# Kernel optimization log

Hardware: AMD Instinct MI355X
Metric: run time of the kernel (lower is better)

The kernel has to match this reference:

```python
import jax, jax.numpy as jnp
import numpy as np

HEAD_DIM = 64
GRID = 4
DS = 4
EPS = 1e-6


def conv1x1(x, w, b):
    # x: (B,C,H,W), w: (O,C), b: (O,)
    return jnp.einsum('bchw,oc->bohw', x, w) + b[None, :, None, None]


def setup_inputs() -> dict:
    key = jax.random.key(0)
    ks = jax.random.split(key, 12)
    B, N, C = 16, 4096, 256
    s = 0.02
    return {
        'x': jax.random.normal(ks[0], (B, N, C), dtype=jnp.float32),
        'w_qkv': s * jax.random.normal(ks[1], (3 * C, C), dtype=jnp.float32),
        'b_qkv': jnp.zeros((3 * C,), dtype=jnp.float32),
        'w_q': s * jax.random.normal(ks[2], (C, C), dtype=jnp.float32),
        'b_q': jnp.zeros((C,), dtype=jnp.float32),
        'w_kv': s * jax.random.normal(ks[3], (2 * C, C), dtype=jnp.float32),
        'b_kv': jnp.zeros((2 * C,), dtype=jnp.float32),
        'w_proj': s * jax.random.normal(ks[4], (C, C), dtype=jnp.float32),
        'b_proj': jnp.zeros((C,), dtype=jnp.float32),
        'gn_w': jnp.ones((C,), dtype=jnp.float32),
        'gn_b': jnp.zeros((C,), dtype=jnp.float32),
    }


def reference(x, w_qkv, b_qkv, w_q, b_q, w_kv, b_kv, w_proj, b_proj, gn_w, gn_b):
    B, N, C = x.shape
    H = W = int(np.sqrt(N))
    hd = HEAD_DIM
    nh = C // hd
    gs = GRID
    scale = hd ** -0.5

    xi = x.transpose(0, 2, 1).reshape(B, C, H, W)
    qkv = conv1x1(xi, w_qkv, b_qkv)  # (B,3C,H,W)

    # ---- grid-window attention (gs x gs windows) ----
    gh, gw = H // gs, W // gs
    qkv = qkv.reshape(B, 3, nh, hd, gh, gs, gw, gs)
    qkv = qkv.transpose(1, 0, 2, 4, 6, 5, 7, 3).reshape(3, -1, gs * gs, hd)
    q, k, v = qkv[0], qkv[1], qkv[2]  # (B*nh*gh*gw, gs*gs, hd)
    attn = jax.nn.softmax(jnp.einsum('wqd,wkd->wqk', q, k) * scale, axis=-1)
    grid_x = jnp.einsum('wqk,wkd->wqd', attn, v)
    grid_x = grid_x.reshape(B, nh, gh, gw, gs, gs, hd)
    grid_x = grid_x.transpose(0, 1, 6, 2, 4, 3, 5).reshape(B, C, H, W)

    # channels_first LayerNorm(x + grid_x)
    z = xi + grid_x
    u = z.mean(1, keepdims=True)
    s2 = ((z - u) ** 2).mean(1, keepdims=True)
    grid_x = gn_w[None, :, None, None] * ((z - u) / jnp.sqrt(s2 + EPS)) + gn_b[None, :, None, None]

    # ---- pooled global attention ----
    qg = conv1x1(grid_x, w_q, b_q).reshape(B, nh, hd, N).transpose(0, 1, 3, 2)  # (B,nh,N,hd)
    pooled = grid_x.reshape(B, C, H // DS, DS, W // DS, DS).mean(axis=(3, 5))
    kv = conv1x1(pooled, w_kv, b_kv).reshape(B, 2, nh, hd, -1).transpose(1, 0, 2, 4, 3)
    k, v = kv[0], kv[1]  # (B,nh,Np,hd)
    attn = jax.nn.softmax(jnp.einsum('bhqd,bhkd->bhqk', qg, k) * scale, axis=-1)
    global_x = jnp.einsum('bhqk,bhkd->bhqd', attn, v)
    global_x = global_x.transpose(0, 1, 3, 2).reshape(B, C, H, W) + grid_x

    out = conv1x1(global_x, w_proj, b_proj)
    return out.reshape(B, C, N).transpose(0, 2, 1)
```

## Files before the change

### kernel.cpp

```cpp
#include <hip/hip_runtime.h>
#include <cstddef>

#define SCALE 0.125f
#define LN_EPS 1e-6f

typedef __attribute__((ext_vector_type(8))) short bf16x8;
typedef __attribute__((ext_vector_type(4))) float f32x4;

__device__ __forceinline__ unsigned short f2bf(float f) {
    unsigned u = __float_as_uint(f);
    return (unsigned short)((u + 0x7FFFu + ((u >> 16) & 1u)) >> 16);
}
__device__ __forceinline__ unsigned pack2(float a, float b) {
    return (unsigned)f2bf(a) | ((unsigned)f2bf(b) << 16);
}
__device__ __forceinline__ float bflo(unsigned v) { return __uint_as_float(v << 16); }
__device__ __forceinline__ float bfhi(unsigned v) { return __uint_as_float(v & 0xFFFF0000u); }
__device__ __forceinline__ float bf2f(short s) { return __uint_as_float(((unsigned)(unsigned short)s) << 16); }

#define GLOAD16(gp, lp) __builtin_amdgcn_global_load_lds( \
    (const __attribute__((address_space(1))) void*)(gp),  \
    (__attribute__((address_space(3))) void*)(lp), 16, 0, 0)

__global__ __launch_bounds__(256) void k_castw(
    const float* __restrict__ wqkv, const float* __restrict__ wq,
    const float* __restrict__ wkv, const float* __restrict__ wproj,
    short* __restrict__ wb)
{
    const int blk = blockIdx.x;
    const float* src; size_t so, doff;
    if (blk < 96)       { src = wqkv;  so = (size_t)blk * 2048;         doff = 0; }
    else if (blk < 128) { src = wq;    so = (size_t)(blk - 96) * 2048;  doff = 196608; }
    else if (blk < 192) { src = wkv;   so = (size_t)(blk - 128) * 2048; doff = 262144; }
    else                { src = wproj; so = (size_t)(blk - 192) * 2048; doff = 393216; }
    const size_t idx = so + (size_t)threadIdx.x * 8;
    const float4 f0 = *(const float4*)(src + idx);
    const float4 f1 = *(const float4*)(src + idx + 4);
    uint4 o;
    o.x = pack2(f0.x, f0.y); o.y = pack2(f0.z, f0.w);
    o.z = pack2(f1.x, f1.y); o.w = pack2(f1.z, f1.w);
    *(uint4*)(wb + doff + idx) = o;
}

__global__ __launch_bounds__(256) void k_castx(
    const float* __restrict__ x, short* __restrict__ xb)
{
    const size_t i = ((size_t)blockIdx.x * 256 + threadIdx.x) * 8;
    const float4 f0 = *(const float4*)(x + i);
    const float4 f1 = *(const float4*)(x + i + 4);
    uint4 o;
    o.x = pack2(f0.x, f0.y); o.y = pack2(f0.z, f0.w);
    o.z = pack2(f1.x, f1.y); o.w = pack2(f1.z, f1.w);
    *(uint4*)(xb + i) = o;
}

template<int OUTMODE>
__global__ __launch_bounds__(256, 4) void k_gemm(
    const short* __restrict__ Asrc, const short* __restrict__ Bw,
    const float* __restrict__ bias, void* __restrict__ Cdst,
    short* __restrict__ Vdst, int ldc, int nbn)
{
    __shared__ short Sh[17408];
    short* const As0 = Sh;
    short* const Bs0 = Sh + 8192;

    const int tid = threadIdx.x;
    const int q8 = gridDim.x >> 3;
    const int bid = (blockIdx.x & 7) * q8 + (blockIdx.x >> 3);
    const int bm = bid / nbn, bn = bid % nbn;
    const size_t m0 = (size_t)bm * 128, n0 = (size_t)bn * 128;
    const int wid = tid >> 6, lane = tid & 63;
    const int wr = wid >> 1, wc = wid & 1;
    const int g = lane >> 4, r = lane & 15;
    const int rowc = lane >> 3, gran = lane & 7;

    f32x4 acc[4][4];
    #pragma unroll
    for (int mi = 0; mi < 4; ++mi)
        #pragma unroll
        for (int nj = 0; nj < 4; ++nj) acc[mi][nj] = (f32x4)0.f;

    auto STAGE = [&](int kt) {
        const int k0 = kt * 64;
        #pragma unroll
        for (int i = 0; i < 4; ++i) {
            const int rbase = wid * 32 + i * 8;
            const int row = rbase + rowc;
            const int sg = gran ^ (row & 7);
            GLOAD16(Asrc + (m0 + row) * 256 + k0 + sg * 8, As0 + rbase * 64);
            GLOAD16(Bw   + (n0 + row) * 256 + k0 + sg * 8, Bs0 + rbase * 64);
        }
    };

    auto COMPUTE = [&]() {
        #pragma unroll
        for (int ks = 0; ks < 2; ++ks) {
            const int ke = ks * 32 + g * 8;
            bf16x8 a[4], b[4];
            #pragma unroll
            for (int mi = 0; mi < 4; ++mi) {
                const int row = wr * 64 + mi * 16 + r;
                a[mi] = *(const bf16x8*)&As0[row * 64 + (ke ^ ((row & 7) << 3))];
            }
            #pragma unroll
            for (int nj = 0; nj < 4; ++nj) {
                const int row = wc * 64 + nj * 16 + r;
                b[nj] = *(const bf16x8*)&Bs0[row * 64 + (ke ^ ((row & 7) << 3))];
            }
            #pragma unroll
            for (int mi = 0; mi < 4; ++mi)
                #pragma unroll
                for (int nj = 0; nj < 4; ++nj)
                    acc[mi][nj] = __builtin_amdgcn_mfma_f32_16x16x32_bf16(
                        a[mi], b[nj], acc[mi][nj], 0, 0, 0);
        }
    };

    #pragma unroll
    for (int kt = 0; kt < 4; ++kt) {
        STAGE(kt);
        __syncthreads();
        COMPUTE();
        __syncthreads();
    }

    if (OUTMODE == 1) {
        short* const Cl = Sh;
        #pragma unroll
        for (int nj = 0; nj < 4; ++nj) {
            const int col = wc * 64 + nj * 16 + r;
            const float bv = bias[n0 + col];
            #pragma unroll
            for (int mi = 0; mi < 4; ++mi) {
                const int row = wr * 64 + mi * 16 + g * 4;
                #pragma unroll
                for (int e = 0; e < 4; ++e)
                    Cl[(row + e) * 136 + col] = (short)f2bf(acc[mi][nj][e] + bv);
            }
        }
        __syncthreads();
        short* C = (short*)Cdst;
        #pragma unroll
        for (int j = 0; j < 8; ++j) {
            const int row = j * 16 + (tid >> 4);
            const int c8 = (tid & 15) * 8;
            const uint4 v = *(const uint4*)&Cl[row * 136 + c8];
            *(uint4*)(C + (m0 + row) * ldc + n0 + c8) = v;
        }
    } else {
        #pragma unroll
        for (int nj = 0; nj < 4; ++nj) {
            const size_t col = n0 + wc * 64 + nj * 16 + r;
            const float bv = bias[col];
            #pragma unroll
            for (int mi = 0; mi < 4; ++mi) {
                const size_t row = m0 + wr * 64 + mi * 16 + g * 4;
                #pragma unroll
                for (int e = 0; e < 4; ++e) {
                    const float v = acc[mi][nj][e] + bv;
                    const size_t rr = row + e;
                    if (OUTMODE == 0) ((float*)Cdst)[rr * ldc + col] = v;
                    else {
                        const int colk = (int)col - 256;
                        if (colk < 0) ((short*)Cdst)[rr * 256 + col] = (short)f2bf(v);
                        else {
                            const int hh = colk >> 6, dd = colk & 63;
                            Vdst[((((rr >> 8) * 4 + hh) * 64 + dd) << 8) + (rr & 255)] = (short)f2bf(v);
                        }
                    }
                }
            }
        }
    }
}

__global__ __launch_bounds__(256) void k_vtr(
    const short* __restrict__ qkvb, short* __restrict__ vwb)
{
    __shared__ short Vl[16][260];
    const int tid = threadIdx.x;
    const int blk = blockIdx.x;
    const int b = blk >> 8, win = blk & 255;
    const int ghi = win >> 4, gwi = win & 15;
    const size_t nb = (size_t)b * 4096;

    #pragma unroll
    for (int i = 0; i < 2; ++i) {
        const int c = i * 256 + tid;
        const int tok = c >> 5, ch = c & 31;
        const int n = (ghi * 4 + (tok >> 2)) * 64 + gwi * 4 + (tok & 3);
        const uint4 u = *(const uint4*)(qkvb + (nb + n) * 768 + 512 + ch * 8);
        short* dst = &Vl[tok][ch * 8];
        *(uint2*)dst = make_uint2(u.x, u.y);
        *(uint2*)(dst + 4) = make_uint2(u.z, u.w);
    }
    __syncthreads();

    unsigned w[8];
    #pragma unroll
    for (int k = 0; k < 8; ++k) {
        const unsigned lo = (unsigned)(unsigned short)Vl[2 * k][tid];
        const unsigned hi = (unsigned)(unsigned short)Vl[2 * k + 1][tid];
        w[k] = lo | (hi << 16);
    }
    short* dst = vwb + ((size_t)blk * 256 + tid) * 16;
    *(uint4*)dst = make_uint4(w[0], w[1], w[2], w[3]);
    *(uint4*)(dst + 8) = make_uint4(w[4], w[5], w[6], w[7]);
}

__global__ __launch_bounds__(256) void k_win3(
    const short* __restrict__ qkvb, const short* __restrict__ vwb,
    const short* __restrict__ xb, const float* __restrict__ gnw,
    const float* __restrict__ gnb, short* __restrict__ lnb,
    short* __restrict__ pooledb)
{
    __shared__ float zbuf[16][260];
    __shared__ short Pb[4][16][40];

    const int tid = threadIdx.x;
    const int blk = blockIdx.x;
    const int b = blk >> 8, win = blk & 255;
    const int ghi = win >> 4, gwi = win & 15;
    const size_t nb = (size_t)b * 4096;
    const int h = tid >> 6, lane = tid & 63;
    const int g = lane >> 4, l15 = lane & 15;

    const int n15 = (ghi * 4 + (l15 >> 2)) * 64 + gwi * 4 + (l15 & 3);
    const size_t qkrow = (nb + n15) * 768;
    const bf16x8 aq0 = *(const bf16x8*)(qkvb + qkrow + h * 64 + g * 8);
    const bf16x8 aq1 = *(const bf16x8*)(qkvb + qkrow + h * 64 + 32 + g * 8);
    const bf16x8 bk0 = *(const bf16x8*)(qkvb + qkrow + 256 + h * 64 + g * 8);
    const bf16x8 bk1 = *(const bf16x8*)(qkvb + qkrow + 256 + h * 64 + 32 + g * 8);

    f32x4 acc = (f32x4)0.f;
    acc = __builtin_amdgcn_mfma_f32_16x16x32_bf16(aq0, bk0, acc, 0, 0, 0);
    acc = __builtin_amdgcn_mfma_f32_16x16x32_bf16(aq1, bk1, acc, 0, 0, 0);

    float p[4];
    #pragma unroll
    for (int e = 0; e < 4; ++e) {
        const float s = acc[e] * SCALE;
        float mm = s;
        mm = fmaxf(mm, __shfl_xor(mm, 1)); mm = fmaxf(mm, __shfl_xor(mm, 2));
        mm = fmaxf(mm, __shfl_xor(mm, 4)); mm = fmaxf(mm, __shfl_xor(mm, 8));
        const float pe = __expf(s - mm);
        float rs = pe;
        rs += __shfl_xor(rs, 1); rs += __shfl_xor(rs, 2);
        rs += __shfl_xor(rs, 4); rs += __shfl_xor(rs, 8);
        p[e] = pe / rs;
    }
    #pragma unroll
    for (int e = 0; e < 4; ++e) {
        Pb[h][g * 4 + e][l15] = (short)f2bf(p[e]);
        Pb[h][g * 4 + e][16 + l15] = 0;
    }
    __syncthreads();

    const bf16x8 ap = *(const bf16x8*)&Pb[h][l15][g * 8];
    f32x4 oc[4];
    #pragma unroll
    for (int nt = 0; nt < 4; ++nt) oc[nt] = (f32x4)0.f;
    const short* vbase = vwb + ((((size_t)b * 256 + win) * 4 + h) << 10);
    #pragma unroll
    for (int nt = 0; nt < 4; ++nt) {
        const bf16x8 bv = *(const bf16x8*)(vbase + (nt * 16 + l15) * 16 + g * 8);
        oc[nt] = __builtin_amdgcn_mfma_f32_16x16x32_bf16(ap, bv, oc[nt], 0, 0, 0);
    }
    #pragma unroll
    for (int e = 0; e < 4; ++e)
        #pragma unroll
        for (int nt = 0; nt < 4; ++nt)
            zbuf[g * 4 + e][h * 64 + nt * 16 + l15] = oc[nt][e];
    __syncthreads();

    {
        const float4 gw = ((const float4*)gnw)[lane];
        const float4 gb = ((const float4*)gnb)[lane];
        #pragma unroll
        for (int i = 0; i < 4; ++i) {
            const int t = h * 4 + i;
            const int n = (ghi * 4 + (t >> 2)) * 64 + gwi * 4 + (t & 3);
            float4 zv = *(const float4*)&zbuf[t][lane * 4];
            const short4 xv = *(const short4*)(xb + (nb + n) * 256 + lane * 4);
            zv.x += bf2f(xv.x); zv.y += bf2f(xv.y);
            zv.z += bf2f(xv.z); zv.w += bf2f(xv.w);
            float ssum = zv.x + zv.y + zv.z + zv.w;
            for (int off = 1; off < 64; off <<= 1) ssum += __shfl_xor(ssum, off);
            const float u = ssum * (1.f / 256.f);
            const float dx = zv.x - u, dy = zv.y - u, dz = zv.z - u, dw = zv.w - u;
            float vsum = dx * dx + dy * dy + dz * dz + dw * dw;
            for (int off = 1; off < 64; off <<= 1) vsum += __shfl_xor(vsum, off);
            const float rinv = rsqrtf(vsum * (1.f / 256.f) + LN_EPS);
            float4 y;
            y.x = gw.x * dx * rinv + gb.x;
            y.y = gw.y * dy * rinv + gb.y;
            y.z = gw.z * dz * rinv + gb.z;
            y.w = gw.w * dw * rinv + gb.w;
            *(float4*)&zbuf[t][lane * 4] = y;
            short4 sv;
            sv.x = (short)f2bf(y.x); sv.y = (short)f2bf(y.y);
            sv.z = (short)f2bf(y.z); sv.w = (short)f2bf(y.w);
            *(short4*)(lnb + (nb + n) * 256 + lane * 4) = sv;
        }
    }
    __syncthreads();

    {
        float ps = 0.f;
        #pragma unroll
        for (int t = 0; t < 16; ++t) ps += zbuf[t][tid];
        pooledb[((size_t)b * 256 + win) * 256 + tid] = (short)f2bf(ps * (1.f / 16.f));
    }
}

#define CP 136
__global__ __launch_bounds__(512, 4) void k_glb(
    const short* __restrict__ qgb, const short* __restrict__ kb,
    const short* __restrict__ vtb, const short* __restrict__ lnb,
    short* __restrict__ gxb)
{
    __shared__ short Ks[128 * 64];
    __shared__ short Vt[64 * 128];
    __shared__ short Pl[8][16 * CP];

    const int tid = threadIdx.x;
    const int bid = (blockIdx.x & 7) * 256 + (blockIdx.x >> 3);
    const int bh = bid >> 5, qt = bid & 31;
    const int b = bh >> 2, h = bh & 3;
    const int q0 = qt * 128;
    const size_t nb = (size_t)b * 4096;

    const int w = tid >> 6, lane = tid & 63;
    const int g = lane >> 4, l15 = lane & 15;

    bf16x8 aq[2];
    {
        const int n = q0 + w * 16 + l15;
        const short* qp = qgb + (nb + n) * 256 + h * 64 + g * 8;
        aq[0] = *(const bf16x8*)qp;
        aq[1] = *(const bf16x8*)(qp + 32);
    }

    f32x4 oc[4];
    #pragma unroll
    for (int nt = 0; nt < 4; ++nt) oc[nt] = (f32x4)0.f;
    float rs[4] = {0.f, 0.f, 0.f, 0.f};

    const short* ksrc = kb + ((size_t)b * 256) * 256 + h * 64;
    const short* vsrc = vtb + (size_t)bh * 16384;
    short* Pw = &Pl[w][0];

    for (int c = 0; c < 2; ++c) {
        if (c) __syncthreads();
        #pragma unroll
        for (int i = 0; i < 2; ++i) {
            const int cc = i * 512 + tid;
            const int p = cc >> 3, d8 = (cc & 7) * 8;
            const uint4 u = *(const uint4*)(ksrc + (size_t)(c * 128 + p) * 256 + d8);
            *(uint4*)&Ks[p * 64 + (d8 ^ ((p & 7) << 3))] = u;
        }
        #pragma unroll
        for (int i = 0; i < 2; ++i) {
            const int cc = i * 512 + tid;
            const int d = cc >> 4, k8 = (cc & 15) * 8;
            const uint4 u = *(const uint4*)(vsrc + d * 256 + c * 128 + k8);
            *(uint4*)&Vt[d * 128 + (k8 ^ ((d & 7) << 3))] = u;
        }
        __syncthreads();

        f32x4 acc[8];
        #pragma unroll
        for (int nt = 0; nt < 8; ++nt) acc[nt] = (f32x4)0.f;
        #pragma unroll
        for (int nt = 0; nt < 8; ++nt) {
            const int key = nt * 16 + l15;
            const int sw = (key & 7) << 3;
            const bf16x8 bk0 = *(const bf16x8*)&Ks[key * 64 + ((g * 8) ^ sw)];
            const bf16x8 bk1 = *(const bf16x8*)&Ks[key * 64 + ((g * 8 + 32) ^ sw)];
            acc[nt] = __builtin_amdgcn_mfma_f32_16x16x32_bf16(aq[0], bk0, acc[nt], 0, 0, 0);
            acc[nt] = __builtin_amdgcn_mfma_f32_16x16x32_bf16(aq[1], bk1, acc[nt], 0, 0, 0);
        }

        #pragma unroll
        for (int e = 0; e < 4; ++e) {
            const int prow = (g * 4 + e) * CP;
            float rsum = 0.f;
            #pragma unroll
            for (int nt = 0; nt < 8; ++nt) {
                const float p = __expf(acc[nt][e] * SCALE);
                rsum += p;
                Pw[prow + nt * 16 + l15] = (short)f2bf(p);
            }
            rs[e] += rsum;
        }

        #pragma unroll
        for (int ks = 0; ks < 4; ++ks) {
            const int kc = ks * 32 + g * 8;
            const bf16x8 a0 = *(const bf16x8*)&Pw[l15 * CP + kc];
            #pragma unroll
            for (int nt = 0; nt < 4; ++nt) {
                const int d = nt * 16 + l15;
                const bf16x8 bv = *(const bf16x8*)&Vt[d * 128 + (kc ^ ((d & 7) << 3))];
                oc[nt] = __builtin_amdgcn_mfma_f32_16x16x32_bf16(a0, bv, oc[nt], 0, 0, 0);
            }
        }
    }

    #pragma unroll
    for (int e = 0; e < 4; ++e) {
        float v = rs[e];
        v += __shfl_xor(v, 1); v += __shfl_xor(v, 2);
        v += __shfl_xor(v, 4); v += __shfl_xor(v, 8);
        rs[e] = v;
    }

    #pragma unroll
    for (int e = 0; e < 4; ++e) {
        const float inv = 1.f / rs[e];
        const int n = q0 + w * 16 + g * 4 + e;
        const size_t base = (nb + n) * 256 + h * 64;
        #pragma unroll
        for (int nt = 0; nt < 4; ++nt) {
            const int d = nt * 16 + l15;
            gxb[base + d] = (short)f2bf(oc[nt][e] * inv + bf2f(lnb[base + d]));
        }
    }
}

extern "C" void kernel_launch(void* const* d_in, const int* in_sizes, int n_in,
                              void* d_out, int out_size, void* d_ws, size_t ws_size,
                              hipStream_t stream)
{
    (void)in_sizes; (void)n_in; (void)out_size; (void)ws_size;
    const float* x     = (const float*)d_in[0];
    const float* wqkv  = (const float*)d_in[1];
    const float* bqkv  = (const float*)d_in[2];
    const float* wq    = (const float*)d_in[3];
    const float* bq    = (const float*)d_in[4];
    const float* wkv   = (const float*)d_in[5];
    const float* bkv   = (const float*)d_in[6];
    const float* wproj = (const float*)d_in[7];
    const float* bproj = (const float*)d_in[8];
    const float* gnw   = (const float*)d_in[9];
    const float* gnb   = (const float*)d_in[10];
    float* out = (float*)d_out;

    char* wsb = (char*)d_ws;
    short* wb      = (short*)(wsb + 0);
    short* qkvb    = (short*)(wsb + 1048576);
    short* lnb     = (short*)(wsb + 101711872);
    short* qgb     = (short*)(wsb + 135266304);
    short* kb      = (short*)(wsb + 168820736);
    short* vtb     = (short*)(wsb + 170917888);
    short* pooledb = (short*)(wsb + 173015040);
    short* gxb     = (short*)(wsb + 175112192);
    short* vwb     = gxb;
    short* xb      = (short*)(wsb + 208666624);

    k_castw<<<dim3(224),  dim3(256), 0, stream>>>(wqkv, wq, wkv, wproj, wb);
    k_castx<<<dim3(8192), dim3(256), 0, stream>>>(x, xb);
    k_gemm<1><<<dim3(3072), dim3(256), 0, stream>>>(xb, wb, bqkv, qkvb, nullptr, 768, 6);
    k_vtr<<<dim3(4096), dim3(256), 0, stream>>>(qkvb, vwb);
    k_win3<<<dim3(4096), dim3(256), 0, stream>>>(qkvb, vwb, xb, gnw, gnb, lnb, pooledb);
    k_gemm<1><<<dim3(1024), dim3(256), 0, stream>>>(lnb, wb + 196608, bq, qgb, nullptr, 256, 2);
    k_gemm<2><<<dim3(128), dim3(256), 0, stream>>>(pooledb, wb + 262144, bkv, kb, vtb, 512, 4);
    k_glb<<<dim3(2048), dim3(512), 0, stream>>>(qgb, kb, vtb, lnb, gxb);
    k_gemm<0><<<dim3(1024), dim3(256), 0, stream>>>(gxb, wb + 393216, bproj, out, nullptr, 256, 2);
}
```

Baseline: 193.3 us.

## Alias K and P tiles in LDS, use direct global-to-LDS loads, raise occupancy

The global attention kernel now places the P staging buffer in the same LDS region as the K tile, with an extra barrier after QK^T so the two can share space. This cuts LDS use enough to raise the occupancy hint from 4 to 6 blocks per CU. K and V tiles are loaded with global_load_lds, applying the XOR swizzle on the source address, and the softmax uses exp2 with a prescaled constant and truncates to bf16 instead of rounding. The extra barrier, the truncation-based rounding, and register pressure at higher occupancy are the trade-offs.

```diff
diff --git a/kernel.cpp b/kernel.cpp
--- a/kernel.cpp
+++ b/kernel.cpp
@@ -2,6 +2,7 @@
 #include <cstddef>
 
 #define SCALE 0.125f
+#define S2E 0.18033688011112042f
 #define LN_EPS 1e-6f
 
 typedef __attribute__((ext_vector_type(8))) short bf16x8;
@@ -314,14 +315,15 @@
 }
 
 #define CP 136
-__global__ __launch_bounds__(512, 4) void k_glb(
+__global__ __launch_bounds__(512, 6) void k_glb(
     const short* __restrict__ qgb, const short* __restrict__ kb,
     const short* __restrict__ vtb, const short* __restrict__ lnb,
     short* __restrict__ gxb)
 {
-    __shared__ short Ks[128 * 64];
-    __shared__ short Vt[64 * 128];
-    __shared__ short Pl[8][16 * CP];
+    __shared__ short Sh2[8192 + 17408];
+    short* const Vt = Sh2;
+    short* const Ks = Sh2 + 8192;
+    short* const Pl = Sh2 + 8192;
 
     const int tid = threadIdx.x;
     const int bid = (blockIdx.x & 7) * 256 + (blockIdx.x >> 3);
@@ -332,6 +334,7 @@
 
     const int w = tid >> 6, lane = tid & 63;
     const int g = lane >> 4, l15 = lane & 15;
+    const int wbase = tid & ~63;
 
     bf16x8 aq[2];
     {
@@ -348,23 +351,25 @@
 
     const short* ksrc = kb + ((size_t)b * 256) * 256 + h * 64;
     const short* vsrc = vtb + (size_t)bh * 16384;
-    short* Pw = &Pl[w][0];
+    short* Pw = Pl + w * (16 * CP);
 
     for (int c = 0; c < 2; ++c) {
         if (c) __syncthreads();
         #pragma unroll
         for (int i = 0; i < 2; ++i) {
             const int cc = i * 512 + tid;
-            const int p = cc >> 3, d8 = (cc & 7) * 8;
-            const uint4 u = *(const uint4*)(ksrc + (size_t)(c * 128 + p) * 256 + d8);
-            *(uint4*)&Ks[p * 64 + (d8 ^ ((p & 7) << 3))] = u;
+            const int p = cc >> 3;
+            const int sg = (cc & 7) ^ (p & 7);
+            GLOAD16(ksrc + (size_t)(c * 128 + p) * 256 + sg * 8,
+                    Ks + (i * 512 + wbase) * 8);
         }
         #pragma unroll
         for (int i = 0; i < 2; ++i) {
             const int cc = i * 512 + tid;
-            const int d = cc >> 4, k8 = (cc & 15) * 8;
-            const uint4 u = *(const uint4*)(vsrc + d * 256 + c * 128 + k8);
-            *(uint4*)&Vt[d * 128 + (k8 ^ ((d & 7) << 3))] = u;
+            const int d = cc >> 4;
+            const int sl = (cc & 15) ^ (d & 7);
+            GLOAD16(vsrc + d * 256 + c * 128 + sl * 8,
+                    Vt + (i * 512 + wbase) * 8);
         }
         __syncthreads();
 
@@ -380,6 +385,7 @@
             acc[nt] = __builtin_amdgcn_mfma_f32_16x16x32_bf16(aq[0], bk0, acc[nt], 0, 0, 0);
             acc[nt] = __builtin_amdgcn_mfma_f32_16x16x32_bf16(aq[1], bk1, acc[nt], 0, 0, 0);
         }
+        __syncthreads();
 
         #pragma unroll
         for (int e = 0; e < 4; ++e) {
@@ -387,9 +393,9 @@
             float rsum = 0.f;
             #pragma unroll
             for (int nt = 0; nt < 8; ++nt) {
-                const float p = __expf(acc[nt][e] * SCALE);
-                rsum += p;
-                Pw[prow + nt * 16 + l15] = (short)f2bf(p);
+                const unsigned up = __float_as_uint(exp2f(acc[nt][e] * S2E));
+                Pw[prow + nt * 16 + l15] = (short)(up >> 16);
+                rsum += __uint_as_float(up & 0xFFFF0000u);
             }
             rs[e] += rsum;
         }
```

After: 217.4 us. 12.4% more time.
